# Kernel tuning notes

Hardware: AMD Instinct MI355X
Metric: run time of the kernel (lower is better)

Reference implementation:

```python
import jax, jax.numpy as jnp
from jax import lax
import numpy as np

KS = 15  # kernel_size
PAD = KS // 2


def setup_inputs() -> dict:
    key = jax.random.key(0)
    k1, _ = jax.random.split(key)
    images = jax.random.uniform(k1, (16, 3, 1024, 1024), dtype=jnp.float32)
    # uniform box filter weight, matches conv.weight.fill_(1/(k*k))
    weight = jnp.ones((1, 1, KS, KS), dtype=jnp.float32)
    return {"images": images, "weight": weight}


def reference(images, weight):
    # channel-wise min over B, G, R channels -> [B, 1, H, W]
    dark = jnp.min(images[:, :3, :, :], axis=1, keepdims=True)
    # 15x15 box average conv, padding=7, no bias
    w = weight * (1.0 / (KS * KS))
    out = lax.conv_general_dilated(
        dark, w,
        window_strides=(1, 1),
        padding=[(PAD, PAD), (PAD, PAD)],
        dimension_numbers=("NCHW", "OIHW", "NCHW"),
    )
    return out
```

## Files before the change

### kernel.cpp

```cpp
#include <hip/hip_runtime.h>

#define KS   15
#define PAD  7
#define TILE 64
#define HI   (TILE + KS - 1)
#define LDW  84
#define NQ   20
#define NIT  (HI * NQ)
#define STR2 68

__global__ __launch_bounds__(256, 6) void dcp_kernel(
    const float* __restrict__ img, const float* __restrict__ weight,
    float* __restrict__ out)
{
    __shared__ float S[HI * LDW];

    const int tid  = threadIdx.x;
    const int wave = tid >> 6;
    const int lane = tid & 63;

    const int bid = blockIdx.x;
    const int swz = (bid & 7) * 512 + (bid >> 3);
    const int b   = swz >> 8;
    const int ty0 = ((swz >> 4) & 15) * TILE;
    const int tx0 = (swz & 15) * TILE;

    const int H = 1024, W = 1024;
    const long long plane = (long long)H * W;
    const float* base = img + (long long)b * 3 * plane;
    const float scale = weight[0] * (1.0f / (KS * KS));

    auto load3 = [&](int it, float4* c) {
        int r  = it / NQ;
        int c4 = it - r * NQ;
        int gy = ty0 + r - PAD;
        int gx = tx0 - 8 + 4 * c4;
        if ((unsigned)gy < (unsigned)H && (unsigned)gx <= (unsigned)(W - 4)) {
            long long off = (long long)gy * W + gx;
            c[0] = *(const float4*)(base + off);
            c[1] = *(const float4*)(base + off + plane);
            c[2] = *(const float4*)(base + off + 2 * plane);
        } else {
            c[0] = c[1] = c[2] = make_float4(0.f, 0.f, 0.f, 0.f);
        }
    };
    auto write_min = [&](int it, const float4* c) {
        int r  = it / NQ;
        int c4 = it - r * NQ;
        float4 v;
        v.x = fminf(c[0].x, fminf(c[1].x, c[2].x));
        v.y = fminf(c[0].y, fminf(c[1].y, c[2].y));
        v.z = fminf(c[0].z, fminf(c[1].z, c[2].z));
        v.w = fminf(c[0].w, fminf(c[1].w, c[2].w));
        *(float4*)(&S[r * LDW + 4 * c4]) = v;
    };

    {
        float4 c0[3], c1[3];
        load3(tid, c0);
        #pragma unroll
        for (int k = 0; k < 5; ++k) {
            load3(tid + 256 * (k + 1), c1);
            write_min(tid + 256 * k, c0);
            c0[0] = c1[0]; c0[1] = c1[1]; c0[2] = c1[2];
        }
        write_min(tid + 256 * 5, c0);
        if (tid < NIT - 1536) {
            load3(1536 + tid, c0);
            write_min(1536 + tid, c0);
        }
    }
    __syncthreads();

    float buf[32] __attribute__((aligned(16)));

    {
        const int rb = wave * 16;
        #pragma unroll
        for (int k = 0; k < 30; ++k) buf[k] = S[(rb + k) * LDW + lane];
        __syncthreads();
        float run = 0.f;
        #pragma unroll
        for (int k = 0; k < 14; ++k) run += buf[k];
        #pragma unroll
        for (int j = 0; j < 16; ++j) {
            run += buf[j + 14];
            S[(rb + j) * LDW + lane] = run;
            run -= buf[j];
        }
    }
    {
        const int rb = wave * 16;
        const int c  = 64 + lane;
        if (lane < 16) {
            #pragma unroll
            for (int k = 0; k < 30; ++k) buf[k] = S[(rb + k) * LDW + c];
        }
        __syncthreads();
        if (lane < 16) {
            float run = 0.f;
            #pragma unroll
            for (int k = 0; k < 14; ++k) run += buf[k];
            #pragma unroll
            for (int j = 0; j < 16; ++j) {
                run += buf[j + 14];
                S[(rb + j) * LDW + c] = run;
                run -= buf[j];
            }
        }
        __syncthreads();
    }

    {
        const int r = lane;
        const int s = wave;
        const int bp = r * LDW + s * 16;
        #pragma unroll
        for (int q = 0; q < 8; ++q)
            *(float4*)(&buf[4 * q]) = *(const float4*)(&S[bp + 4 * q]);
        float o[16];
        float run = 0.f;
        #pragma unroll
        for (int k = 1; k <= 14; ++k) run += buf[k];
        #pragma unroll
        for (int j = 0; j < 16; ++j) {
            run += buf[j + 15];
            o[j] = run * scale;
            run -= buf[j + 1];
        }
        __syncthreads();
        #pragma unroll
        for (int q = 0; q < 4; ++q)
            *(float4*)(&S[r * STR2 + s * 16 + 4 * q]) =
                make_float4(o[4 * q], o[4 * q + 1], o[4 * q + 2], o[4 * q + 3]);
    }
    __syncthreads();

    {
        float* obase = out + (long long)b * plane + (long long)ty0 * W + tx0;
        #pragma unroll
        for (int k = 0; k < 4; ++k) {
            const int qi  = tid + 256 * k;
            const int row = qi >> 4;
            const int qc  = qi & 15;
            float4 v = *(const float4*)(&S[row * STR2 + 4 * qc]);
            *(float4*)(obase + (long long)row * W + 4 * qc) = v;
        }
    }
}

extern "C" void kernel_launch(void* const* d_in, const int* in_sizes, int n_in,
                              void* d_out, int out_size, void* d_ws, size_t ws_size,
                              hipStream_t stream) {
    const float* img    = (const float*)d_in[0];
    const float* weight = (const float*)d_in[1];
    float* out = (float*)d_out;

    dim3 grid(4096);
    dim3 block(256);
    dcp_kernel<<<grid, block, 0, stream>>>(img, weight, out);
}
```

Before: 53.33 us.

## Process two tiles per block, prefetching second tile's loads during first's compute

Each block now handles two horizontally adjacent 64x64 tiles, and the grid is halved. Global loads and the channel-min for the second tile are issued while the first tile's separable box-filter passes and output store run, so memory latency overlaps with LDS compute. Output stores switch to nontemporal. The cost is more live registers (the prefetched float4s), which may hurt occupancy under launch_bounds(256,6), and halo loads are no longer shared between the two tiles.

```diff
diff --git a/kernel.cpp b/kernel.cpp
--- a/kernel.cpp
+++ b/kernel.cpp
@@ -9,6 +9,8 @@
 #define NIT  (HI * NQ)
 #define STR2 68
 
+typedef float f32x4 __attribute__((ext_vector_type(4)));
+
 __global__ __launch_bounds__(256, 6) void dcp_kernel(
     const float* __restrict__ img, const float* __restrict__ weight,
     float* __restrict__ out)
@@ -19,22 +21,25 @@
     const int wave = tid >> 6;
     const int lane = tid & 63;
 
-    const int bid = blockIdx.x;
-    const int swz = (bid & 7) * 512 + (bid >> 3);
-    const int b   = swz >> 8;
-    const int ty0 = ((swz >> 4) & 15) * TILE;
-    const int tx0 = (swz & 15) * TILE;
+    const int bid  = blockIdx.x;
+    const int swzL = (bid & 7) * 256 + (bid >> 3);
+    const int L0   = swzL * 2;
 
     const int H = 1024, W = 1024;
     const long long plane = (long long)H * W;
+
+    const int b   = L0 >> 8;
+    const int ty0 = ((L0 >> 4) & 15) * TILE;
+    const int tx0 = (L0 & 15) * TILE;
+    const int tx1 = tx0 + TILE;
     const float* base = img + (long long)b * 3 * plane;
     const float scale = weight[0] * (1.0f / (KS * KS));
 
-    auto load3 = [&](int it, float4* c) {
+    auto load3 = [&](int tx, int it, float4* c) {
         int r  = it / NQ;
         int c4 = it - r * NQ;
         int gy = ty0 + r - PAD;
-        int gx = tx0 - 8 + 4 * c4;
+        int gx = tx - 8 + 4 * c4;
         if ((unsigned)gy < (unsigned)H && (unsigned)gx <= (unsigned)(W - 4)) {
             long long off = (long long)gy * W + gx;
             c[0] = *(const float4*)(base + off);
@@ -44,37 +49,23 @@
             c[0] = c[1] = c[2] = make_float4(0.f, 0.f, 0.f, 0.f);
         }
     };
-    auto write_min = [&](int it, const float4* c) {
-        int r  = it / NQ;
-        int c4 = it - r * NQ;
+    auto min3 = [](const float4* c) -> float4 {
         float4 v;
         v.x = fminf(c[0].x, fminf(c[1].x, c[2].x));
         v.y = fminf(c[0].y, fminf(c[1].y, c[2].y));
         v.z = fminf(c[0].z, fminf(c[1].z, c[2].z));
         v.w = fminf(c[0].w, fminf(c[1].w, c[2].w));
+        return v;
+    };
+    auto dswrite = [&](int it, float4 v) {
+        int r  = it / NQ;
+        int c4 = it - r * NQ;
         *(float4*)(&S[r * LDW + 4 * c4]) = v;
     };
 
-    {
-        float4 c0[3], c1[3];
-        load3(tid, c0);
-        #pragma unroll
-        for (int k = 0; k < 5; ++k) {
-            load3(tid + 256 * (k + 1), c1);
-            write_min(tid + 256 * k, c0);
-            c0[0] = c1[0]; c0[1] = c1[1]; c0[2] = c1[2];
-        }
-        write_min(tid + 256 * 5, c0);
-        if (tid < NIT - 1536) {
-            load3(1536 + tid, c0);
-            write_min(1536 + tid, c0);
-        }
-    }
-    __syncthreads();
-
     float buf[32] __attribute__((aligned(16)));
 
-    {
+    auto p2a = [&]() {
         const int rb = wave * 16;
         #pragma unroll
         for (int k = 0; k < 30; ++k) buf[k] = S[(rb + k) * LDW + lane];
@@ -88,8 +79,8 @@
             S[(rb + j) * LDW + lane] = run;
             run -= buf[j];
         }
-    }
-    {
+    };
+    auto p2b = [&]() {
         const int rb = wave * 16;
         const int c  = 64 + lane;
         if (lane < 16) {
@@ -109,11 +100,10 @@
             }
         }
         __syncthreads();
-    }
-
-    {
-        const int r = lane;
-        const int s = wave;
+    };
+    auto p3 = [&]() {
+        const int r  = lane;
+        const int s  = wave;
         const int bp = r * LDW + s * 16;
         #pragma unroll
         for (int q = 0; q < 8; ++q)
@@ -133,20 +123,62 @@
         for (int q = 0; q < 4; ++q)
             *(float4*)(&S[r * STR2 + s * 16 + 4 * q]) =
                 make_float4(o[4 * q], o[4 * q + 1], o[4 * q + 2], o[4 * q + 3]);
-    }
-    __syncthreads();
-
-    {
-        float* obase = out + (long long)b * plane + (long long)ty0 * W + tx0;
+        __syncthreads();
+    };
+    auto p4 = [&](int txx) {
+        float* obase = out + (long long)b * plane + (long long)ty0 * W + txx;
         #pragma unroll
         for (int k = 0; k < 4; ++k) {
             const int qi  = tid + 256 * k;
             const int row = qi >> 4;
             const int qc  = qi & 15;
-            float4 v = *(const float4*)(&S[row * STR2 + 4 * qc]);
-            *(float4*)(obase + (long long)row * W + 4 * qc) = v;
+            f32x4 v = *(const f32x4*)(&S[row * STR2 + 4 * qc]);
+            __builtin_nontemporal_store(v, (f32x4*)(obase + (long long)row * W + 4 * qc));
         }
+    };
+
+    {
+        float4 c0[3], c1[3];
+        load3(tx0, tid, c0);
+        #pragma unroll
+        for (int k = 0; k < 5; ++k) {
+            load3(tx0, tid + 256 * (k + 1), c1);
+            dswrite(tid + 256 * k, min3(c0));
+            c0[0] = c1[0]; c0[1] = c1[1]; c0[2] = c1[2];
+        }
+        dswrite(tid + 256 * 5, min3(c0));
+        if (tid < NIT - 1536) { load3(tx0, 1536 + tid, c0); dswrite(1536 + tid, min3(c0)); }
     }
+    __syncthreads();
+
+    float4 A0[3], A1[3];
+    float4 dark[7];
+    load3(tx1, tid,        A0);
+    load3(tx1, tid + 256,  A1);
+    p2a();
+    dark[0] = min3(A0); dark[1] = min3(A1);
+    load3(tx1, tid + 512,  A0);
+    load3(tx1, tid + 768,  A1);
+    p2b();
+    dark[2] = min3(A0); dark[3] = min3(A1);
+    load3(tx1, tid + 1024, A0);
+    load3(tx1, tid + 1280, A1);
+    p3();
+    dark[4] = min3(A0); dark[5] = min3(A1);
+    if (tid < 24) load3(tx1, 1536 + tid, A0);
+    p4(tx0);
+    dark[6] = min3(A0);
+    __syncthreads();
+
+    #pragma unroll
+    for (int k = 0; k < 6; ++k) dswrite(tid + 256 * k, dark[k]);
+    if (tid < 24) dswrite(1536 + tid, dark[6]);
+    __syncthreads();
+
+    p2a();
+    p2b();
+    p3();
+    p4(tx1);
 }
 
 extern "C" void kernel_launch(void* const* d_in, const int* in_sizes, int n_in,
@@ -156,7 +188,7 @@
     const float* weight = (const float*)d_in[1];
     float* out = (float*)d_out;
 
-    dim3 grid(4096);
+    dim3 grid(2048);
     dim3 block(256);
     dcp_kernel<<<grid, block, 0, stream>>>(img, weight, out);
 }
```

After: 120.3 us. 126% more time.
